# Performance work log

Hardware: AMD Instinct MI355X
Metric: run time of the kernel (lower is better)

The kernel has to match this reference:

```python
import jax, jax.numpy as jnp
import numpy as np

NEG = -9e15
SLOPE = 0.1  # LeakyReLU negative_slope in the torch module

B, N, NFEAT = 4, 2048, 256
NHID, NHEADS, NOUT = 64, 8, 128


def setup_inputs() -> dict:
    key = jax.random.key(0)
    ks = jax.random.split(key, 8)
    x = jax.random.normal(ks[0], (B, N, NFEAT), dtype=jnp.float32)
    adj = jax.random.randint(ks[1], (B, N, N), 0, 2, dtype=jnp.int32)
    s = 0.1
    Wh = jax.random.normal(ks[2], (NHEADS, NFEAT, NHID), dtype=jnp.float32) * s
    ah = jax.random.normal(ks[3], (NHEADS, 2 * NHID), dtype=jnp.float32) * s
    bh = jax.random.normal(ks[4], (NHEADS, NHID), dtype=jnp.float32) * s
    Wo = jax.random.normal(ks[5], (NHID * NHEADS, NOUT), dtype=jnp.float32) * s
    ao = jax.random.normal(ks[6], (2 * NOUT,), dtype=jnp.float32) * s
    bo = jax.random.normal(ks[7], (NOUT,), dtype=jnp.float32) * s
    return {"x": x, "adj": adj, "Wh": Wh, "ah": ah, "bh": bh,
            "Wo": Wo, "ao": ao, "bo": bo}


def _leaky(v):
    return jnp.where(v >= 0, v, SLOPE * v)


def _gat_layer(x, adj, W, a, b):
    # x: [B,N,Fin], W: [Fin,F], a: [2F], b: [F]
    h = jnp.einsum('bnf,fo->bno', x, W)          # [B,N,F]
    F = W.shape[1]
    a1, a2 = a[:F], a[F:]
    s1 = h @ a1                                   # [B,N] (query / row term)
    s2 = h @ a2                                   # [B,N] (key / col term)
    e = _leaky(s1[:, :, None] + s2[:, None, :])   # [B,N,N], avoids a_input blowup
    e = jnp.where(adj > 0, e, NEG)
    att = jax.nn.softmax(e, axis=2)               # [B,N,N]
    h_prime = jnp.einsum('bnm,bmf->bnf', att, h) + b
    return jax.nn.elu(h_prime)


def reference(x, adj, Wh, ah, bh, Wo, ao, bo):
    # per-head layers, vmapped over the head axis of the stacked params
    heads = jax.vmap(lambda W, a, b: _gat_layer(x, adj, W, a, b))(Wh, ah, bh)
    # [H,B,N,F] -> concat heads along feature dim: [B,N,H*F]
    hcat = jnp.transpose(heads, (1, 2, 0, 3)).reshape(x.shape[0], x.shape[1], -1)
    out = _gat_layer(hcat, adj, Wo, ao, bo)
    return jax.nn.relu(out)
```

## Files before the change

kernel.cpp:

```cpp
#include <hip/hip_runtime.h>

constexpr int B_ = 4;
constexpr int N_ = 2048;
constexpr int NFEAT_ = 256;
constexpr int NHEADS_ = 8;
constexpr float SLOPE_ = 0.1f;
constexpr float L2E = 1.4426950408889634f;

typedef __attribute__((ext_vector_type(8))) __fp16 f16x8;
typedef __attribute__((ext_vector_type(4))) __fp16 f16x4;
typedef __attribute__((ext_vector_type(2))) __fp16 f16x2;
typedef __attribute__((ext_vector_type(4))) float f32x4;
typedef __attribute__((ext_vector_type(2))) float f32x2;

__device__ __forceinline__ f16x8 pack8(const float* v) {
  union { f16x2 h2[4]; f16x8 h8; } u;
  u.h2[0] = __builtin_amdgcn_cvt_pkrtz(v[0], v[1]);
  u.h2[1] = __builtin_amdgcn_cvt_pkrtz(v[2], v[3]);
  u.h2[2] = __builtin_amdgcn_cvt_pkrtz(v[4], v[5]);
  u.h2[3] = __builtin_amdgcn_cvt_pkrtz(v[6], v[7]);
  return u.h8;
}
__device__ __forceinline__ f16x4 pack4(float a, float b, float c, float d) {
  union { f16x2 h2[2]; f16x4 h4; } u;
  u.h2[0] = __builtin_amdgcn_cvt_pkrtz(a, b);
  u.h2[1] = __builtin_amdgcn_cvt_pkrtz(c, d);
  return u.h4;
}

__device__ __forceinline__ unsigned int wpair(f32x2 p2, f32x2 s2p,
                                              f16x2 sl2, f16x2 cq2,
                                              unsigned int pm) {
  f32x2 z;
  asm("v_pk_add_f32 %0, %1, %2" : "=v"(z) : "v"(p2), "v"(s2p));
  f16x2 t0 = __builtin_amdgcn_cvt_pkrtz(z.x, z.y);
  f16x2 t1, tm;
  asm("v_pk_fma_f16 %0, %1, %2, %3" : "=v"(t1) : "v"(sl2), "v"(t0), "v"(cq2));
  asm("v_pk_max_f16 %0, %1, %2" : "=v"(tm) : "v"(t0), "v"(t1));
  unsigned int utm;
  __builtin_memcpy(&utm, &tm, 4);
  unsigned int hi, elo, ehi, pk;
  asm("v_lshrrev_b32 %0, 16, %1" : "=v"(hi) : "v"(utm));
  asm("v_exp_f16 %0, %1" : "=v"(elo) : "v"(utm));
  asm("v_exp_f16 %0, %1" : "=v"(ehi) : "v"(hi));
  asm("v_pack_b32_f16 %0, %1, %2" : "=v"(pk) : "v"(elo), "v"(ehi));
  return pk & pm;
}

__global__ __launch_bounds__(256) void k_prep(
    const int* __restrict__ adj, unsigned short* __restrict__ mask2,
    const float* __restrict__ Wh, __fp16* __restrict__ WhB,
    const float* __restrict__ Wo, __fp16* __restrict__ WoB)
{
  const int bid = blockIdx.x;
  const int l = threadIdx.x & 63;
  if (bid < 4096) {
    const size_t gw = ((size_t)bid * 256 + threadIdx.x) >> 6;
    const int jt = (int)(gw & 31);
    const int ig16 = (int)((gw >> 5) & 127);
    const int b = (int)(gw >> 12);
    const int q = l >> 4, c15 = l & 15;
    const int* base = adj + ((size_t)b * N_ + ig16 * 16) * N_ + jt * 64 + l;
    unsigned int msk = 0;
    #pragma unroll
    for (int r = 0; r < 16; ++r) {
      int a = base[(size_t)r * N_];
      unsigned long long bal = __ballot(a > 0);
      unsigned int v = (unsigned int)((bal >> (q * 8)) & 0xffull)
                     | ((unsigned int)((bal >> (q * 8 + 32)) & 0xffull) << 8);
      if (r == c15) msk = v;
    }
    mask2[gw * 64 + l] = (unsigned short)msk;
  } else if (bid < 4160) {
    int s = (int)(((bid - 4096) * 256 + threadIdx.x) >> 6);
    int h = s >> 5, ks = (s >> 2) & 7, ft = s & 3;
    const float* src = Wh + ((size_t)h * 256 + ks * 32 + (l >> 4) * 8) * 64 + ft * 16 + (l & 15);
    float v[8];
    #pragma unroll
    for (int j = 0; j < 8; ++j) v[j] = src[(size_t)j * 64];
    *(f16x8*)(WhB + (size_t)s * 512 + l * 8) = pack8(v);
  } else {
    int s = (int)(((bid - 4160) * 256 + threadIdx.x) >> 6);
    int ks = s >> 3, ft = s & 7;
    const float* src = Wo + ((size_t)ks * 32 + (l >> 4) * 8) * 128 + ft * 16 + (l & 15);
    float v[8];
    #pragma unroll
    for (int j = 0; j < 8; ++j) v[j] = src[(size_t)j * 128];
    *(f16x8*)(WoB + (size_t)s * 512 + l * 8) = pack8(v);
  }
}

__global__ __launch_bounds__(256, 4) void k_gemm1(
    const float* __restrict__ x, const __fp16* __restrict__ WhB,
    const float* __restrict__ ah,
    __fp16* __restrict__ hB1, float* __restrict__ s1h, float* __restrict__ s2h)
{
  constexpr int XP = 264;
  __shared__ __fp16 xs[16 * XP];
  __shared__ __fp16 hT[512 * 16];

  const int t = threadIdx.x;
  const int bid = blockIdx.x;
  const int b = bid >> 7;
  const int n0 = (bid & 127) * 16;

  {
    int r = t >> 4, k0 = (t & 15) * 16;
    const float* src = x + ((size_t)(b * N_) + n0 + r) * NFEAT_ + k0;
    float v0[8], v1[8];
    *(float4*)&v0[0] = *(const float4*)(src);
    *(float4*)&v0[4] = *(const float4*)(src + 4);
    *(float4*)&v1[0] = *(const float4*)(src + 8);
    *(float4*)&v1[4] = *(const float4*)(src + 12);
    *(f16x8*)&xs[r * XP + k0] = pack8(v0);
    *(f16x8*)&xs[r * XP + k0 + 8] = pack8(v1);
  }
  __syncthreads();

  const int w = t >> 6, l = t & 63;
  const int quad = l >> 4, c15 = l & 15;

  f32x4 acc[8];
  #pragma unroll
  for (int i = 0; i < 8; ++i) acc[i] = (f32x4){0.f, 0.f, 0.f, 0.f};

  for (int ks = 0; ks < 8; ++ks) {
    f16x8 af = *(const f16x8*)&xs[c15 * XP + ks * 32 + quad * 8];
    #pragma unroll
    for (int tt = 0; tt < 8; ++tt) {
      int hl = tt >> 2, ft = tt & 3;
      f16x8 bf = *(const f16x8*)(WhB +
          ((((size_t)(2 * w + hl) * 8 + ks) * 4 + ft) * 512) + l * 8);
      acc[tt] = __builtin_amdgcn_mfma_f32_16x16x32_f16(af, bf, acc[tt], 0, 0, 0);
    }
  }

  #pragma unroll
  for (int hl = 0; hl < 2; ++hl) {
    int head = 2 * w + hl;
    float a1v[4], a2v[4];
    #pragma unroll
    for (int ft = 0; ft < 4; ++ft) {
      a1v[ft] = ah[head * 128 + ft * 16 + c15] * L2E;
      a2v[ft] = ah[head * 128 + 64 + ft * 16 + c15] * L2E;
    }
    #pragma unroll
    for (int r = 0; r < 4; ++r) {
      float v1 = 0.f, v2 = 0.f;
      #pragma unroll
      for (int ft = 0; ft < 4; ++ft) {
        v1 = fmaf(acc[hl * 4 + ft][r], a1v[ft], v1);
        v2 = fmaf(acc[hl * 4 + ft][r], a2v[ft], v2);
      }
      #pragma unroll
      for (int off = 1; off < 16; off <<= 1) {
        v1 += __shfl_xor(v1, off, 64);
        v2 += __shfl_xor(v2, off, 64);
      }
      if (c15 == 0) {
        s1h[(size_t)(b * NHEADS_ + head) * N_ + n0 + quad * 4 + r] = v1;
        s2h[(size_t)(b * NHEADS_ + head) * N_ + n0 + quad * 4 + r] = v2;
      }
    }
  }

  #pragma unroll
  for (int tt = 0; tt < 8; ++tt) {
    int f = (2 * w + (tt >> 2)) * 64 + (tt & 3) * 16 + c15;
    *(f16x4*)&hT[f * 16 + quad * 4] =
        pack4(acc[tt][0], acc[tt][1], acc[tt][2], acc[tt][3]);
  }
  __syncthreads();

  const int base_oct = (n0 >> 3) & 3;
  #pragma unroll
  for (int q = 0; q < 4; ++q) {
    int s = t + q * 256;
    int c15v = s & 15, oct = (s >> 4) & 1, ft = (s >> 5) & 3, head = s >> 7;
    f16x8 v = *(const f16x8*)&hT[(head * 64 + ft * 16 + c15v) * 16 + oct * 8];
    int lane0 = (base_oct + oct) * 16 + c15v;
    *(f16x8*)(hB1 +
        ((((size_t)(b * NHEADS_ + head) * 64 + (n0 >> 5)) * 4 + ft) * 512) + lane0 * 8) = v;
  }
}

__global__ __launch_bounds__(256, 4) void k_gemm2(
    const __fp16* __restrict__ g1, const __fp16* __restrict__ WoB,
    const float* __restrict__ ao,
    __fp16* __restrict__ hB2, float* __restrict__ s1o, float* __restrict__ s2o)
{
  constexpr int GP = 520;
  __shared__ __fp16 gs[16 * GP];
  __shared__ __fp16 hT[128 * 16];
  __shared__ float sd1[4][16], sd2[4][16];

  const int t = threadIdx.x;
  const int bid = blockIdx.x;
  const int b = bid >> 7;
  const int n0 = (bid & 127) * 16;

  {
    int r = t >> 4, k0 = (t & 15) * 32;
    const __fp16* src = g1 + ((size_t)(b * N_) + n0 + r) * 512 + k0;
    #pragma unroll
    for (int i = 0; i < 4; ++i)
      *(f16x8*)&gs[r * GP + k0 + i * 8] = *(const f16x8*)(src + i * 8);
  }
  __syncthreads();

  const int w = t >> 6, l = t & 63;
  const int quad = l >> 4, c15 = l & 15;

  f32x4 acc[2];
  acc[0] = (f32x4){0.f, 0.f, 0.f, 0.f};
  acc[1] = (f32x4){0.f, 0.f, 0.f, 0.f};

  for (int ks = 0; ks < 16; ++ks) {
    f16x8 af = *(const f16x8*)&gs[c15 * GP + ks * 32 + quad * 8];
    #pragma unroll
    for (int tt = 0; tt < 2; ++tt) {
      int ft = 2 * w + tt;
      f16x8 bf = *(const f16x8*)(WoB + (((size_t)ks * 8 + ft) * 512) + l * 8);
      acc[tt] = __builtin_amdgcn_mfma_f32_16x16x32_f16(af, bf, acc[tt], 0, 0, 0);
    }
  }

  {
    float a1v[2], a2v[2];
    #pragma unroll
    for (int tt = 0; tt < 2; ++tt) {
      int f = (2 * w + tt) * 16 + c15;
      a1v[tt] = ao[f] * L2E;
      a2v[tt] = ao[128 + f] * L2E;
    }
    #pragma unroll
    for (int r = 0; r < 4; ++r) {
      float v1 = acc[0][r] * a1v[0] + acc[1][r] * a1v[1];
      float v2 = acc[0][r] * a2v[0] + acc[1][r] * a2v[1];
      #pragma unroll
      for (int off = 1; off < 16; off <<= 1) {
        v1 += __shfl_xor(v1, off, 64);
        v2 += __shfl_xor(v2, off, 64);
      }
      if (c15 == 0) { sd1[w][quad * 4 + r] = v1; sd2[w][quad * 4 + r] = v2; }
    }
  }

  #pragma unroll
  for (int tt = 0; tt < 2; ++tt) {
    int f = (2 * w + tt) * 16 + c15;
    *(f16x4*)&hT[f * 16 + quad * 4] =
        pack4(acc[tt][0], acc[tt][1], acc[tt][2], acc[tt][3]);
  }
  __syncthreads();

  if (t < 16)
    s1o[(size_t)b * N_ + n0 + t] = sd1[0][t] + sd1[1][t] + sd1[2][t] + sd1[3][t];
  else if (t < 32) {
    int rr = t - 16;
    s2o[(size_t)b * N_ + n0 + rr] = sd2[0][rr] + sd2[1][rr] + sd2[2][rr] + sd2[3][rr];
  }

  {
    int c15v = t & 15, oct = (t >> 4) & 1, ft = t >> 5;
    f16x8 v = *(const f16x8*)&hT[(ft * 16 + c15v) * 16 + oct * 8];
    int base_oct = (n0 >> 3) & 3;
    int lane0 = (base_oct + oct) * 16 + c15v;
    *(f16x8*)(hB2 +
        (((size_t)(b * 64 + (n0 >> 5)) * 8 + ft) * 512) + lane0 * 8) = v;
  }
}

__global__ __launch_bounds__(512, 4) void k_att1(
    const __fp16* __restrict__ hB, const float* __restrict__ s1,
    const float* __restrict__ s2, const unsigned short* __restrict__ mask2,
    const float* __restrict__ bias, __fp16* __restrict__ g1)
{
  constexpr int NRG = 4, NJQ = 2, JLEN = 1024, TJ = 32, NIT = JLEN / TJ;
  constexpr int TILE = TJ * 64;

  __shared__ __fp16 vbuf[NJQ][2][TILE];
  __shared__ float s2s[N_];
  __shared__ float red[8];
  __shared__ uint2 mlut[16];

  const int tid = threadIdx.x;
  const int w = tid >> 6, l = tid & 63;
  const int quad = l >> 4, c15 = l & 15;
  const int rowg = w % NRG, jq = w / NRG;
  const int tc = rowg * 64 + l;

  int idx = blockIdx.x;
  const int ig = idx & 31; idx >>= 5;
  const int head = idx & 7;
  const int b = idx >> 3;
  const int i0w = ig * 64 + rowg * 16;

  const float* s1p = s1 + (size_t)(b * 8 + head) * N_;
  const float* s2p = s2 + (size_t)(b * 8 + head) * N_;
  const char* hBp = (const char*)(hB + (size_t)(b * 8 + head) * (N_ / 32) * 2048);
  const unsigned short* mp = mask2 + ((size_t)(b * 128 + (i0w >> 4)) * 32) * 64 + l;

  const int jbase = jq * JLEN;

  if (tid < 16) {
    unsigned int v = tid;
    mlut[tid] = (uint2){ ((v & 1u) ? 0xffffu : 0u) | ((v & 2u) ? 0xffff0000u : 0u),
                         ((v & 4u) ? 0xffffu : 0u) | ((v & 8u) ? 0xffff0000u : 0u) };
  }

  float4 pf0 = *(const float4*)(hBp + (size_t)(jbase >> 5) * 4096 + tc * 16);
  unsigned short mk = mp[(size_t)(jbase >> 6) * 64];

  float4 sv = *(const float4*)(s2p + tid * 4);
  *(float4*)&s2s[tid * 4] = sv;
  float lm = fmaxf(fmaxf(sv.x, sv.y), fmaxf(sv.z, sv.w));
  #pragma unroll
  for (int off = 1; off < 64; off <<= 1) lm = fmaxf(lm, __shfl_xor(lm, off, 64));
  if (l == 0) red[w] = lm;
  const float s1v = s1p[i0w + c15];
  *(float4*)((char*)&vbuf[jq][0][0] + tc * 16) = pf0;
  __syncthreads();
  float s2m = red[0];
  #pragma unroll
  for (int q = 1; q < 8; ++q) s2m = fmaxf(s2m, red[q]);

  const float zm = s1v + s2m;
  const float m = fmaxf(zm, SLOPE_ * zm);
  const float p = s1v - m;
  const float cq = (SLOPE_ - 1.f) * m;
  const f16x2 cq2 = __builtin_amdgcn_cvt_pkrtz(cq, cq);
  const f16x2 sl2 = (f16x2){(__fp16)SLOPE_, (__fp16)SLOPE_};
  const f32x2 p2 = {p, p};

  f16x8 ones;
  #pragma unroll
  for (int i = 0; i < 8; ++i) ones[i] = (__fp16)1.0f;

  f32x4 acc[4], acc5;
  #pragma unroll
  for (int t = 0; t < 4; ++t) acc[t] = (f32x4){0.f, 0.f, 0.f, 0.f};
  acc5 = (f32x4){0.f, 0.f, 0.f, 0.f};

  for (int it = 0; it < NIT; ++it) {
    const int cur = it & 1;
    const int j0 = jbase + it * TJ;
    unsigned short nk = 0;
    float4 npf;
    if (it + 1 < NIT) {
      npf = *(const float4*)(hBp + (size_t)((j0 + TJ) >> 5) * 4096 + tc * 16);
      nk = mp[(size_t)((j0 + TJ) >> 6) * 64];
    }

    float4 sA = *(const float4*)&s2s[j0 + quad * 8];
    float4 sB = *(const float4*)&s2s[j0 + quad * 8 + 4];
    const unsigned int mbyte = ((unsigned int)mk >> (8 * ((j0 >> 5) & 1))) & 0xffu;
    const uint2 mA = mlut[mbyte & 15u];
    const uint2 mB = mlut[mbyte >> 4];
    union { unsigned int u[4]; f16x8 v8; } af;
    af.u[0] = wpair(p2, (f32x2){sA.x, sA.y}, sl2, cq2, mA.x);
    af.u[1] = wpair(p2, (f32x2){sA.z, sA.w}, sl2, cq2, mA.y);
    af.u[2] = wpair(p2, (f32x2){sB.x, sB.y}, sl2, cq2, mB.x);
    af.u[3] = wpair(p2, (f32x2){sB.z, sB.w}, sl2, cq2, mB.y);
    const f16x8 a = af.v8;
    acc5 = __builtin_amdgcn_mfma_f32_16x16x32_f16(a, ones, acc5, 0, 0, 0);
    const __fp16* vb = &vbuf[jq][cur][0];
    #pragma unroll
    for (int t = 0; t < 4; ++t) {
      f16x8 bf = *(const f16x8*)(vb + t * 512 + l * 8);
      acc[t] = __builtin_amdgcn_mfma_f32_16x16x32_f16(a, bf, acc[t], 0, 0, 0);
    }

    if (it + 1 < NIT) {
      *(float4*)((char*)&vbuf[jq][cur ^ 1][0] + tc * 16) = npf;
    }
    mk = nk;
    __syncthreads();
  }

  auto pacc = (float(*)[16][64])(&vbuf[0][0][0]);
  auto pls  = (float(*)[16])(&s2s[0]);
  if (jq == 1) {
    #pragma unroll
    for (int t = 0; t < 4; ++t)
      #pragma unroll
      for (int r = 0; r < 4; ++r)
        pacc[rowg][quad * 4 + r][t * 16 + c15] = acc[t][r];
    if (c15 == 0) {
      #pragma unroll
      for (int r = 0; r < 4; ++r) pls[rowg][quad * 4 + r] = acc5[r];
    }
  }
  __syncthreads();
  if (jq == 0) {
    float Lrow[4];
    #pragma unroll
    for (int r = 0; r < 4; ++r)
      Lrow[r] = acc5[r] + pls[rowg][quad * 4 + r];
    #pragma unroll
    for (int t = 0; t < 4; ++t)
      #pragma unroll
      for (int r = 0; r < 4; ++r)
        acc[t][r] += pacc[rowg][quad * 4 + r][t * 16 + c15];
    float lr[4];
    #pragma unroll
    for (int r = 0; r < 4; ++r) lr[r] = 1.f / Lrow[r];
    #pragma unroll
    for (int t = 0; t < 4; ++t) {
      const float bv = bias[head * 64 + t * 16 + c15];
      #pragma unroll
      for (int r = 0; r < 4; ++r) {
        const int i = i0w + quad * 4 + r;
        float v = acc[t][r] * lr[r] + bv;
        v = (v > 0.f) ? v : expm1f(v);
        g1[(size_t)(b * N_ + i) * 512 + head * 64 + t * 16 + c15] = (__fp16)v;
      }
    }
  }
}

__global__ __launch_bounds__(512, 4) void k_att2(
    const __fp16* __restrict__ hB, const float* __restrict__ s1,
    const float* __restrict__ s2, const unsigned short* __restrict__ mask2,
    const float* __restrict__ bias, float* __restrict__ out)
{
  constexpr int NRG = 2, NJQ = 4, JLEN = 512, TJ = 32, NIT = JLEN / TJ;
  constexpr int TILE = TJ * 64;

  __shared__ __fp16 vbuf[NJQ][2][TILE];
  __shared__ float s2s[N_];
  __shared__ float red[8];
  __shared__ uint2 mlut[16];

  const int tid = threadIdx.x;
  const int w = tid >> 6, l = tid & 63;
  const int quad = l >> 4, c15 = l & 15;
  const int rowg = w % NRG, jq = w / NRG;
  const int tc = rowg * 64 + l;

  int idx = blockIdx.x;
  const int ig = idx & 63; idx >>= 6;
  const int fs = idx & 1;
  const int b = idx >> 1;
  const int i0w = ig * 32 + rowg * 16;

  const float* s1p = s1 + (size_t)b * N_;
  const float* s2p = s2 + (size_t)b * N_;
  const char* hBp = (const char*)(hB + (size_t)b * 64 * 4096 + fs * 2048);
  const unsigned short* mp = mask2 + ((size_t)(b * 128 + (i0w >> 4)) * 32) * 64 + l;

  const int jbase = jq * JLEN;

  if (tid < 16) {
    unsigned int v = tid;
    mlut[tid] = (uint2){ ((v & 1u) ? 0xffffu : 0u) | ((v & 2u) ? 0xffff0000u : 0u),
                         ((v & 4u) ? 0xffffu : 0u) | ((v & 8u) ? 0xffff0000u : 0u) };
  }

  float4 pf0, pf1;
  {
    const char* srcb = hBp + (size_t)(jbase >> 5) * 8192;
    pf0 = *(const float4*)(srcb + tc * 16);
    pf1 = *(const float4*)(srcb + (tc + 128) * 16);
  }
  unsigned short mk = mp[(size_t)(jbase >> 6) * 64];

  float4 sv = *(const float4*)(s2p + tid * 4);
  *(float4*)&s2s[tid * 4] = sv;
  float lm = fmaxf(fmaxf(sv.x, sv.y), fmaxf(sv.z, sv.w));
  #pragma unroll
  for (int off = 1; off < 64; off <<= 1) lm = fmaxf(lm, __shfl_xor(lm, off, 64));
  if (l == 0) red[w] = lm;
  const float s1v = s1p[i0w + c15];
  *(float4*)((char*)&vbuf[jq][0][0] + tc * 16) = pf0;
  *(float4*)((char*)&vbuf[jq][0][0] + (tc + 128) * 16) = pf1;
  __syncthreads();
  float s2m = red[0];
  #pragma unroll
  for (int q = 1; q < 8; ++q) s2m = fmaxf(s2m, red[q]);

  const float zm = s1v + s2m;
  const float m = fmaxf(zm, SLOPE_ * zm);
  const float p = s1v - m;
  const float cq = (SLOPE_ - 1.f) * m;
  const f16x2 cq2 = __builtin_amdgcn_cvt_pkrtz(cq, cq);
  const f16x2 sl2 = (f16x2){(__fp16)SLOPE_, (__fp16)SLOPE_};
  const f32x2 p2 = {p, p};

  f16x8 ones;
  #pragma unroll
  for (int i = 0; i < 8; ++i) ones[i] = (__fp16)1.0f;

  f32x4 acc[4], acc5;
  #pragma unroll
  for (int t = 0; t < 4; ++t) acc[t] = (f32x4){0.f, 0.f, 0.f, 0.f};
  acc5 = (f32x4){0.f, 0.f, 0.f, 0.f};

  for (int it = 0; it < NIT; ++it) {
    const int cur = it & 1;
    const int j0 = jbase + it * TJ;
    unsigned short nk = 0;
    float4 npf0, npf1;
    if (it + 1 < NIT) {
      const char* srcb = hBp + (size_t)((j0 + TJ) >> 5) * 8192;
      npf0 = *(const float4*)(srcb + tc * 16);
      npf1 = *(const float4*)(srcb + (tc + 128) * 16);
      nk = mp[(size_t)((j0 + TJ) >> 6) * 64];
    }

    float4 sA = *(const float4*)&s2s[j0 + quad * 8];
    float4 sB = *(const float4*)&s2s[j0 + quad * 8 + 4];
    const unsigned int mbyte = ((unsigned int)mk >> (8 * ((j0 >> 5) & 1))) & 0xffu;
    const uint2 mA = mlut[mbyte & 15u];
    const uint2 mB = mlut[mbyte >> 4];
    union { unsigned int u[4]; f16x8 v8; } af;
    af.u[0] = wpair(p2, (f32x2){sA.x, sA.y}, sl2, cq2, mA.x);
    af.u[1] = wpair(p2, (f32x2){sA.z, sA.w}, sl2, cq2, mA.y);
    af.u[2] = wpair(p2, (f32x2){sB.x, sB.y}, sl2, cq2, mB.x);
    af.u[3] = wpair(p2, (f32x2){sB.z, sB.w}, sl2, cq2, mB.y);
    const f16x8 a = af.v8;
    acc5 = __builtin_amdgcn_mfma_f32_16x16x32_f16(a, ones, acc5, 0, 0, 0);
    const __fp16* vb = &vbuf[jq][cur][0];
    #pragma unroll
    for (int t = 0; t < 4; ++t) {
      f16x8 bf = *(const f16x8*)(vb + t * 512 + l * 8);
      acc[t] = __builtin_amdgcn_mfma_f32_16x16x32_f16(a, bf, acc[t], 0, 0, 0);
    }

    if (it + 1 < NIT) {
      char* dst = (char*)&vbuf[jq][cur ^ 1][0];
      *(float4*)(dst + tc * 16) = npf0;
      *(float4*)(dst + (tc + 128) * 16) = npf1;
    }
    mk = nk;
    __syncthreads();
  }

  auto pacc = (float(*)[NRG][16][64])(&vbuf[0][0][0]);
  auto pls  = (float(*)[NRG][16])(&s2s[0]);
  if (jq > 0) {
    #pragma unroll
    for (int t = 0; t < 4; ++t)
      #pragma unroll
      for (int r = 0; r < 4; ++r)
        pacc[jq - 1][rowg][quad * 4 + r][t * 16 + c15] = acc[t][r];
    if (c15 == 0) {
      #pragma unroll
      for (int r = 0; r < 4; ++r) pls[jq - 1][rowg][quad * 4 + r] = acc5[r];
    }
  }
  __syncthreads();
  if (jq == 0) {
    float Lrow[4];
    #pragma unroll
    for (int r = 0; r < 4; ++r) Lrow[r] = acc5[r];
    #pragma unroll
    for (int q = 0; q < NJQ - 1; ++q) {
      #pragma unroll
      for (int t = 0; t < 4; ++t)
        #pragma unroll
        for (int r = 0; r < 4; ++r)
          acc[t][r] += pacc[q][rowg][quad * 4 + r][t * 16 + c15];
      #pragma unroll
      for (int r = 0; r < 4; ++r) Lrow[r] += pls[q][rowg][quad * 4 + r];
    }
    float lr[4];
    #pragma unroll
    for (int r = 0; r < 4; ++r) lr[r] = 1.f / Lrow[r];
    #pragma unroll
    for (int t = 0; t < 4; ++t) {
      const float bv = bias[fs * 64 + t * 16 + c15];
      #pragma unroll
      for (int r = 0; r < 4; ++r) {
        const int i = i0w + quad * 4 + r;
        float v = acc[t][r] * lr[r] + bv;
        out[(size_t)(b * N_ + i) * 128 + fs * 64 + t * 16 + c15] = fmaxf(v, 0.f);
      }
    }
  }
}

extern "C" void kernel_launch(void* const* d_in, const int* in_sizes, int n_in,
                              void* d_out, int out_size, void* d_ws, size_t ws_size,
                              hipStream_t stream) {
  const float* x   = (const float*)d_in[0];
  const int*   adj = (const int*)d_in[1];
  const float* Wh  = (const float*)d_in[2];
  const float* ah  = (const float*)d_in[3];
  const float* bh  = (const float*)d_in[4];
  const float* Wo  = (const float*)d_in[5];
  const float* ao  = (const float*)d_in[6];
  const float* bo  = (const float*)d_in[7];
  float* out = (float*)d_out;

  float* ws   = (float*)d_ws;
  float* s1h  = ws;
  float* s2h  = s1h  + (size_t)B_ * NHEADS_ * N_;
  float* s1o  = s2h  + (size_t)B_ * NHEADS_ * N_;
  float* s2o  = s1o  + (size_t)B_ * N_;
  __fp16* g1  = (__fp16*)(s2o + (size_t)B_ * N_);
  __fp16* hB1 = g1  + (size_t)B_ * N_ * 512;
  __fp16* hB2 = hB1 + (size_t)B_ * NHEADS_ * N_ * 64;
  __fp16* WhB = hB2 + (size_t)B_ * N_ * 128;
  __fp16* WoB = WhB + (size_t)8 * 256 * 64;
  unsigned short* mask2 = (unsigned short*)(WoB + (size_t)512 * 128);

  k_prep<<<4192, 256, 0, stream>>>(adj, mask2, Wh, WhB, Wo, WoB);
  k_gemm1<<<B_ * (N_ / 16), 256, 0, stream>>>(x, WhB, ah, hB1, s1h, s2h);
  k_att1<<<B_ * NHEADS_ * (N_ / 64), 512, 0, stream>>>(
      hB1, s1h, s2h, mask2, bh, g1);
  k_gemm2<<<B_ * (N_ / 16), 256, 0, stream>>>(g1, WoB, ao, hB2, s1o, s2o);
  k_att2<<<B_ * 2 * (N_ / 32), 512, 0, stream>>>(
      hB2, s1o, s2o, mask2, bo, out);
}
```

Baseline: 194.0 us.

## Factor leaky-softmax exponent into per-row and per-column exp products

The attention kernels no longer evaluate exp(leaky(s1+s2)-m) per element. They precompute exp(s2) and exp(slope*s2) per column in fp16 inside the GEMM kernels, and per-row factors exp(s1-m) and exp(slope*s1-m). The inner loop then forms each weight as the max of two packed fp16 products, using monotonicity of exp. The global column max now comes from atomicMax on order-preserving encoded floats, which removes the in-block reduction. k_att1 doubles its j-tile and both attention kernels prefetch the value tile two iterations ahead. This trades per-element exp work for fp16 products whose factors may underflow or overflow, and adds a dependency on atomics that are zeroed in k_prep.

```diff
diff --git a/kernel.cpp b/kernel.cpp
--- a/kernel.cpp
+++ b/kernel.cpp
@@ -11,7 +11,6 @@
 typedef __attribute__((ext_vector_type(4))) __fp16 f16x4;
 typedef __attribute__((ext_vector_type(2))) __fp16 f16x2;
 typedef __attribute__((ext_vector_type(4))) float f32x4;
-typedef __attribute__((ext_vector_type(2))) float f32x2;
 
 __device__ __forceinline__ f16x8 pack8(const float* v) {
   union { f16x2 h2[4]; f16x8 h8; } u;
@@ -28,29 +27,34 @@
   return u.h4;
 }
 
-__device__ __forceinline__ unsigned int wpair(f32x2 p2, f32x2 s2p,
-                                              f16x2 sl2, f16x2 cq2,
-                                              unsigned int pm) {
-  f32x2 z;
-  asm("v_pk_add_f32 %0, %1, %2" : "=v"(z) : "v"(p2), "v"(s2p));
-  f16x2 t0 = __builtin_amdgcn_cvt_pkrtz(z.x, z.y);
-  f16x2 t1, tm;
-  asm("v_pk_fma_f16 %0, %1, %2, %3" : "=v"(t1) : "v"(sl2), "v"(t0), "v"(cq2));
-  asm("v_pk_max_f16 %0, %1, %2" : "=v"(tm) : "v"(t0), "v"(t1));
-  unsigned int utm;
-  __builtin_memcpy(&utm, &tm, 4);
-  unsigned int hi, elo, ehi, pk;
-  asm("v_lshrrev_b32 %0, 16, %1" : "=v"(hi) : "v"(utm));
-  asm("v_exp_f16 %0, %1" : "=v"(elo) : "v"(utm));
-  asm("v_exp_f16 %0, %1" : "=v"(ehi) : "v"(hi));
-  asm("v_pack_b32_f16 %0, %1, %2" : "=v"(pk) : "v"(elo), "v"(ehi));
-  return pk & pm;
+__device__ __forceinline__ unsigned int fenc(float x) {
+  int i = __float_as_int(x);
+  return (i >= 0) ? ((unsigned int)i | 0x80000000u) : (unsigned int)(~i);
+}
+__device__ __forceinline__ float fdec(unsigned int k) {
+  int i = (k & 0x80000000u) ? (int)(k & 0x7fffffffu) : ~(int)k;
+  return __int_as_float(i);
+}
+
+__device__ __forceinline__ unsigned int wmax(f16x2 Ep2, f16x2 Eq2,
+                                             unsigned int e1p, unsigned int e2p) {
+  f16x2 ea, eb;
+  __builtin_memcpy(&ea, &e1p, 4);
+  __builtin_memcpy(&eb, &e2p, 4);
+  f16x2 a, b, c;
+  asm("v_pk_mul_f16 %0, %1, %2" : "=v"(a) : "v"(Ep2), "v"(ea));
+  asm("v_pk_mul_f16 %0, %1, %2" : "=v"(b) : "v"(Eq2), "v"(eb));
+  asm("v_pk_max_f16 %0, %1, %2" : "=v"(c) : "v"(a), "v"(b));
+  unsigned int r;
+  __builtin_memcpy(&r, &c, 4);
+  return r;
 }
 
 __global__ __launch_bounds__(256) void k_prep(
     const int* __restrict__ adj, unsigned short* __restrict__ mask2,
     const float* __restrict__ Wh, __fp16* __restrict__ WhB,
-    const float* __restrict__ Wo, __fp16* __restrict__ WoB)
+    const float* __restrict__ Wo, __fp16* __restrict__ WoB,
+    unsigned int* __restrict__ mxb)
 {
   const int bid = blockIdx.x;
   const int l = threadIdx.x & 63;
@@ -80,6 +84,7 @@
     for (int j = 0; j < 8; ++j) v[j] = src[(size_t)j * 64];
     *(f16x8*)(WhB + (size_t)s * 512 + l * 8) = pack8(v);
   } else {
+    if (bid == 4191 && threadIdx.x < 36) mxb[threadIdx.x] = 0u;
     int s = (int)(((bid - 4160) * 256 + threadIdx.x) >> 6);
     int ks = s >> 3, ft = s & 7;
     const float* src = Wo + ((size_t)ks * 32 + (l >> 4) * 8) * 128 + ft * 16 + (l & 15);
@@ -93,7 +98,9 @@
 __global__ __launch_bounds__(256, 4) void k_gemm1(
     const float* __restrict__ x, const __fp16* __restrict__ WhB,
     const float* __restrict__ ah,
-    __fp16* __restrict__ hB1, float* __restrict__ s1h, float* __restrict__ s2h)
+    __fp16* __restrict__ hB1, float* __restrict__ s1h,
+    __fp16* __restrict__ e1h, __fp16* __restrict__ e2h,
+    unsigned int* __restrict__ mxb)
 {
   constexpr int XP = 264;
   __shared__ __fp16 xs[16 * XP];
@@ -144,6 +151,7 @@
       a1v[ft] = ah[head * 128 + ft * 16 + c15] * L2E;
       a2v[ft] = ah[head * 128 + 64 + ft * 16 + c15] * L2E;
     }
+    float hmax = -1e30f;
     #pragma unroll
     for (int r = 0; r < 4; ++r) {
       float v1 = 0.f, v2 = 0.f;
@@ -158,10 +166,16 @@
         v2 += __shfl_xor(v2, off, 64);
       }
       if (c15 == 0) {
-        s1h[(size_t)(b * NHEADS_ + head) * N_ + n0 + quad * 4 + r] = v1;
-        s2h[(size_t)(b * NHEADS_ + head) * N_ + n0 + quad * 4 + r] = v2;
+        const size_t nn = (size_t)(b * NHEADS_ + head) * N_ + n0 + quad * 4 + r;
+        s1h[nn] = v1;
+        e1h[nn] = (__fp16)__builtin_amdgcn_exp2f(v2);
+        e2h[nn] = (__fp16)__builtin_amdgcn_exp2f(SLOPE_ * v2);
       }
-    }
+      hmax = fmaxf(hmax, v2);
+    }
+    hmax = fmaxf(hmax, __shfl_xor(hmax, 16, 64));
+    hmax = fmaxf(hmax, __shfl_xor(hmax, 32, 64));
+    if (l == 0) atomicMax(&mxb[b * NHEADS_ + head], fenc(hmax));
   }
 
   #pragma unroll
@@ -187,7 +201,9 @@
 __global__ __launch_bounds__(256, 4) void k_gemm2(
     const __fp16* __restrict__ g1, const __fp16* __restrict__ WoB,
     const float* __restrict__ ao,
-    __fp16* __restrict__ hB2, float* __restrict__ s1o, float* __restrict__ s2o)
+    __fp16* __restrict__ hB2, float* __restrict__ s1o,
+    __fp16* __restrict__ e1o, __fp16* __restrict__ e2o,
+    unsigned int* __restrict__ mxb)
 {
   constexpr int GP = 520;
   __shared__ __fp16 gs[16 * GP];
@@ -258,7 +274,15 @@
     s1o[(size_t)b * N_ + n0 + t] = sd1[0][t] + sd1[1][t] + sd1[2][t] + sd1[3][t];
   else if (t < 32) {
     int rr = t - 16;
-    s2o[(size_t)b * N_ + n0 + rr] = sd2[0][rr] + sd2[1][rr] + sd2[2][rr] + sd2[3][rr];
+    float v = sd2[0][rr] + sd2[1][rr] + sd2[2][rr] + sd2[3][rr];
+    e1o[(size_t)b * N_ + n0 + rr] = (__fp16)__builtin_amdgcn_exp2f(v);
+    e2o[(size_t)b * N_ + n0 + rr] = (__fp16)__builtin_amdgcn_exp2f(SLOPE_ * v);
+    float hm = v;
+    hm = fmaxf(hm, __shfl_xor(hm, 1, 64));
+    hm = fmaxf(hm, __shfl_xor(hm, 2, 64));
+    hm = fmaxf(hm, __shfl_xor(hm, 4, 64));
+    hm = fmaxf(hm, __shfl_xor(hm, 8, 64));
+    if (rr == 0) atomicMax(&mxb[32 + b], fenc(hm));
   }
 
   {
@@ -273,15 +297,16 @@
 
 __global__ __launch_bounds__(512, 4) void k_att1(
     const __fp16* __restrict__ hB, const float* __restrict__ s1,
-    const float* __restrict__ s2, const unsigned short* __restrict__ mask2,
+    const __fp16* __restrict__ e1, const __fp16* __restrict__ e2,
+    const unsigned int* __restrict__ mxb,
+    const unsigned short* __restrict__ mask2,
     const float* __restrict__ bias, __fp16* __restrict__ g1)
 {
-  constexpr int NRG = 4, NJQ = 2, JLEN = 1024, TJ = 32, NIT = JLEN / TJ;
+  constexpr int NRG = 4, NJQ = 2, JLEN = 1024, TJ = 64, NIT = JLEN / TJ;
   constexpr int TILE = TJ * 64;
 
   __shared__ __fp16 vbuf[NJQ][2][TILE];
-  __shared__ float s2s[N_];
-  __shared__ float red[8];
+  __shared__ __fp16 ets[2][N_];
   __shared__ uint2 mlut[16];
 
   const int tid = threadIdx.x;
@@ -295,10 +320,10 @@
   const int head = idx & 7;
   const int b = idx >> 3;
   const int i0w = ig * 64 + rowg * 16;
-
-  const float* s1p = s1 + (size_t)(b * 8 + head) * N_;
-  const float* s2p = s2 + (size_t)(b * 8 + head) * N_;
-  const char* hBp = (const char*)(hB + (size_t)(b * 8 + head) * (N_ / 32) * 2048);
+  const int bh = b * NHEADS_ + head;
+
+  const float* s1p = s1 + (size_t)bh * N_;
+  const char* hBp = (const char*)(hB + (size_t)bh * (N_ / 32) * 2048);
   const unsigned short* mp = mask2 + ((size_t)(b * 128 + (i0w >> 4)) * 32) * 64 + l;
 
   const int jbase = jq * JLEN;
@@ -309,29 +334,30 @@
                          ((v & 4u) ? 0xffffu : 0u) | ((v & 8u) ? 0xffff0000u : 0u) };
   }
 
-  float4 pf0 = *(const float4*)(hBp + (size_t)(jbase >> 5) * 4096 + tc * 16);
+  float4 pA0 = *(const float4*)(hBp + (size_t)(jbase >> 5) * 4096 + tc * 16);
+  float4 pA1 = *(const float4*)(hBp + (size_t)(jbase >> 5) * 4096 + (tc + 256) * 16);
+  float4 pB0 = *(const float4*)(hBp + (size_t)((jbase + TJ) >> 5) * 4096 + tc * 16);
+  float4 pB1 = *(const float4*)(hBp + (size_t)((jbase + TJ) >> 5) * 4096 + (tc + 256) * 16);
   unsigned short mk = mp[(size_t)(jbase >> 6) * 64];
 
-  float4 sv = *(const float4*)(s2p + tid * 4);
-  *(float4*)&s2s[tid * 4] = sv;
-  float lm = fmaxf(fmaxf(sv.x, sv.y), fmaxf(sv.z, sv.w));
-  #pragma unroll
-  for (int off = 1; off < 64; off <<= 1) lm = fmaxf(lm, __shfl_xor(lm, off, 64));
-  if (l == 0) red[w] = lm;
+  {
+    const int half = tid >> 8, off = (tid & 255) * 8;
+    const __fp16* src = (half ? e2 : e1) + (size_t)bh * N_ + off;
+    *(f16x8*)&ets[half][off] = *(const f16x8*)src;
+  }
+
   const float s1v = s1p[i0w + c15];
-  *(float4*)((char*)&vbuf[jq][0][0] + tc * 16) = pf0;
-  __syncthreads();
-  float s2m = red[0];
-  #pragma unroll
-  for (int q = 1; q < 8; ++q) s2m = fmaxf(s2m, red[q]);
+  const float s2m = fdec(mxb[bh]);
+  *(float4*)((char*)&vbuf[jq][0][0] + tc * 16) = pA0;
+  *(float4*)((char*)&vbuf[jq][0][0] + (tc + 256) * 16) = pA1;
+  __syncthreads();
 
   const float zm = s1v + s2m;
   const float m = fmaxf(zm, SLOPE_ * zm);
-  const float p = s1v - m;
-  const float cq = (SLOPE_ - 1.f) * m;
-  const f16x2 cq2 = __builtin_amdgcn_cvt_pkrtz(cq, cq);
-  const f16x2 sl2 = (f16x2){(__fp16)SLOPE_, (__fp16)SLOPE_};
-  const f32x2 p2 = {p, p};
+  const float Ep = __builtin_amdgcn_exp2f(s1v - m);
+  const float Eq = __builtin_amdgcn_exp2f(SLOPE_ * s1v - m);
+  const f16x2 Ep2 = __builtin_amdgcn_cvt_pkrtz(Ep, Ep);
+  const f16x2 Eq2 = __builtin_amdgcn_cvt_pkrtz(Eq, Eq);
 
   f16x8 ones;
   #pragma unroll
@@ -345,41 +371,45 @@
   for (int it = 0; it < NIT; ++it) {
     const int cur = it & 1;
     const int j0 = jbase + it * TJ;
+    if (it + 1 < NIT) {
+      *(float4*)((char*)&vbuf[jq][cur ^ 1][0] + tc * 16) = pB0;
+      *(float4*)((char*)&vbuf[jq][cur ^ 1][0] + (tc + 256) * 16) = pB1;
+    }
+    if (it + 2 < NIT) {
+      pB0 = *(const float4*)(hBp + (size_t)((j0 + 2 * TJ) >> 5) * 4096 + tc * 16);
+      pB1 = *(const float4*)(hBp + (size_t)((j0 + 2 * TJ) >> 5) * 4096 + (tc + 256) * 16);
+    }
     unsigned short nk = 0;
-    float4 npf;
-    if (it + 1 < NIT) {
-      npf = *(const float4*)(hBp + (size_t)((j0 + TJ) >> 5) * 4096 + tc * 16);
-      nk = mp[(size_t)((j0 + TJ) >> 6) * 64];
-    }
-
-    float4 sA = *(const float4*)&s2s[j0 + quad * 8];
-    float4 sB = *(const float4*)&s2s[j0 + quad * 8 + 4];
-    const unsigned int mbyte = ((unsigned int)mk >> (8 * ((j0 >> 5) & 1))) & 0xffu;
-    const uint2 mA = mlut[mbyte & 15u];
-    const uint2 mB = mlut[mbyte >> 4];
-    union { unsigned int u[4]; f16x8 v8; } af;
-    af.u[0] = wpair(p2, (f32x2){sA.x, sA.y}, sl2, cq2, mA.x);
-    af.u[1] = wpair(p2, (f32x2){sA.z, sA.w}, sl2, cq2, mA.y);
-    af.u[2] = wpair(p2, (f32x2){sB.x, sB.y}, sl2, cq2, mB.x);
-    af.u[3] = wpair(p2, (f32x2){sB.z, sB.w}, sl2, cq2, mB.y);
-    const f16x8 a = af.v8;
-    acc5 = __builtin_amdgcn_mfma_f32_16x16x32_f16(a, ones, acc5, 0, 0, 0);
-    const __fp16* vb = &vbuf[jq][cur][0];
-    #pragma unroll
-    for (int t = 0; t < 4; ++t) {
-      f16x8 bf = *(const f16x8*)(vb + t * 512 + l * 8);
-      acc[t] = __builtin_amdgcn_mfma_f32_16x16x32_f16(a, bf, acc[t], 0, 0, 0);
-    }
-
-    if (it + 1 < NIT) {
-      *(float4*)((char*)&vbuf[jq][cur ^ 1][0] + tc * 16) = npf;
+    if (it + 1 < NIT) nk = mp[(size_t)((j0 + TJ) >> 6) * 64];
+
+    #pragma unroll
+    for (int h = 0; h < 2; ++h) {
+      const int jk = j0 + h * 32;
+      uint4 e1u = *(const uint4*)((const char*)&ets[0][jk] + quad * 16);
+      uint4 e2u = *(const uint4*)((const char*)&ets[1][jk] + quad * 16);
+      const unsigned int mbyte = ((unsigned int)mk >> (8 * h)) & 0xffu;
+      const uint2 mA = mlut[mbyte & 15u];
+      const uint2 mB = mlut[mbyte >> 4];
+      union { unsigned int u[4]; f16x8 v8; } af;
+      af.u[0] = wmax(Ep2, Eq2, e1u.x, e2u.x) & mA.x;
+      af.u[1] = wmax(Ep2, Eq2, e1u.y, e2u.y) & mA.y;
+      af.u[2] = wmax(Ep2, Eq2, e1u.z, e2u.z) & mB.x;
+      af.u[3] = wmax(Ep2, Eq2, e1u.w, e2u.w) & mB.y;
+      const f16x8 a = af.v8;
+      acc5 = __builtin_amdgcn_mfma_f32_16x16x32_f16(a, ones, acc5, 0, 0, 0);
+      const __fp16* vb = &vbuf[jq][cur][h * 2048];
+      #pragma unroll
+      for (int t = 0; t < 4; ++t) {
+        f16x8 bf = *(const f16x8*)(vb + t * 512 + l * 8);
+        acc[t] = __builtin_amdgcn_mfma_f32_16x16x32_f16(a, bf, acc[t], 0, 0, 0);
+      }
     }
     mk = nk;
     __syncthreads();
   }
 
   auto pacc = (float(*)[16][64])(&vbuf[0][0][0]);
-  auto pls  = (float(*)[16])(&s2s[0]);
+  auto pls  = (float(*)[16])((char*)&vbuf[0][0][0] + 16384);
   if (jq == 1) {
     #pragma unroll
     for (int t = 0; t < 4; ++t)
@@ -421,15 +451,16 @@
 
 __global__ __launch_bounds__(512, 4) void k_att2(
     const __fp16* __restrict__ hB, const float* __restrict__ s1,
-    const float* __restrict__ s2, const unsigned short* __restrict__ mask2,
+    const __fp16* __restrict__ e1, const __fp16* __restrict__ e2,
+    const unsigned int* __restrict__ mxb,
+    const unsigned short* __restrict__ mask2,
     const float* __restrict__ bias, float* __restrict__ out)
 {
   constexpr int NRG = 2, NJQ = 4, JLEN = 512, TJ = 32, NIT = JLEN / TJ;
   constexpr int TILE = TJ * 64;
 
   __shared__ __fp16 vbuf[NJQ][2][TILE];
-  __shared__ float s2s[N_];
-  __shared__ float red[8];
+  __shared__ __fp16 ets[2][N_];
   __shared__ uint2 mlut[16];
 
   const int tid = threadIdx.x;
@@ -445,7 +476,6 @@
   const int i0w = ig * 32 + rowg * 16;
 
   const float* s1p = s1 + (size_t)b * N_;
-  const float* s2p = s2 + (size_t)b * N_;
   const char* hBp = (const char*)(hB + (size_t)b * 64 * 4096 + fs * 2048);
   const unsigned short* mp = mask2 + ((size_t)(b * 128 + (i0w >> 4)) * 32) * 64 + l;
 
@@ -457,35 +487,30 @@
                          ((v & 4u) ? 0xffffu : 0u) | ((v & 8u) ? 0xffff0000u : 0u) };
   }
 
-  float4 pf0, pf1;
+  float4 pA0 = *(const float4*)(hBp + (size_t)(jbase >> 5) * 8192 + tc * 16);
+  float4 pA1 = *(const float4*)(hBp + (size_t)(jbase >> 5) * 8192 + (tc + 128) * 16);
+  float4 pB0 = *(const float4*)(hBp + (size_t)((jbase + TJ) >> 5) * 8192 + tc * 16);
+  float4 pB1 = *(const float4*)(hBp + (size_t)((jbase + TJ) >> 5) * 8192 + (tc + 128) * 16);
+  unsigned short mk = mp[(size_t)(jbase >> 6) * 64];
+
   {
-    const char* srcb = hBp + (size_t)(jbase >> 5) * 8192;
-    pf0 = *(const float4*)(srcb + tc * 16);
-    pf1 = *(const float4*)(srcb + (tc + 128) * 16);
-  }
-  unsigned short mk = mp[(size_t)(jbase >> 6) * 64];
-
-  float4 sv = *(const float4*)(s2p + tid * 4);
-  *(float4*)&s2s[tid * 4] = sv;
-  float lm = fmaxf(fmaxf(sv.x, sv.y), fmaxf(sv.z, sv.w));
-  #pragma unroll
-  for (int off = 1; off < 64; off <<= 1) lm = fmaxf(lm, __shfl_xor(lm, off, 64));
-  if (l == 0) red[w] = lm;
+    const int half = tid >> 8, off = (tid & 255) * 8;
+    const __fp16* src = (half ? e2 : e1) + (size_t)b * N_ + off;
+    *(f16x8*)&ets[half][off] = *(const f16x8*)src;
+  }
+
   const float s1v = s1p[i0w + c15];
-  *(float4*)((char*)&vbuf[jq][0][0] + tc * 16) = pf0;
-  *(float4*)((char*)&vbuf[jq][0][0] + (tc + 128) * 16) = pf1;
-  __syncthreads();
-  float s2m = red[0];
-  #pragma unroll
-  for (int q = 1; q < 8; ++q) s2m = fmaxf(s2m, red[q]);
+  const float s2m = fdec(mxb[32 + b]);
+  *(float4*)((char*)&vbuf[jq][0][0] + tc * 16) = pA0;
+  *(float4*)((char*)&vbuf[jq][0][0] + (tc + 128) * 16) = pA1;
+  __syncthreads();
 
   const float zm = s1v + s2m;
   const float m = fmaxf(zm, SLOPE_ * zm);
-  const float p = s1v - m;
-  const float cq = (SLOPE_ - 1.f) * m;
-  const f16x2 cq2 = __builtin_amdgcn_cvt_pkrtz(cq, cq);
-  const f16x2 sl2 = (f16x2){(__fp16)SLOPE_, (__fp16)SLOPE_};
-  const f32x2 p2 = {p, p};
+  const float Ep = __builtin_amdgcn_exp2f(s1v - m);
+  const float Eq = __builtin_amdgcn_exp2f(SLOPE_ * s1v - m);
+  const f16x2 Ep2 = __builtin_amdgcn_cvt_pkrtz(Ep, Ep);
+  const f16x2 Eq2 = __builtin_amdgcn_cvt_pkrtz(Eq, Eq);
 
   f16x8 ones;
   #pragma unroll
@@ -499,25 +524,27 @@
   for (int it = 0; it < NIT; ++it) {
     const int cur = it & 1;
     const int j0 = jbase + it * TJ;
+    if (it + 1 < NIT) {
+      *(float4*)((char*)&vbuf[jq][cur ^ 1][0] + tc * 16) = pB0;
+      *(float4*)((char*)&vbuf[jq][cur ^ 1][0] + (tc + 128) * 16) = pB1;
+    }
+    if (it + 2 < NIT) {
+      pB0 = *(const float4*)(hBp + (size_t)((j0 + 2 * TJ) >> 5) * 8192 + tc * 16);
+      pB1 = *(const float4*)(hBp + (size_t)((j0 + 2 * TJ) >> 5) * 8192 + (tc + 128) * 16);
+    }
     unsigned short nk = 0;
-    float4 npf0, npf1;
-    if (it + 1 < NIT) {
-      const char* srcb = hBp + (size_t)((j0 + TJ) >> 5) * 8192;
-      npf0 = *(const float4*)(srcb + tc * 16);
-      npf1 = *(const float4*)(srcb + (tc + 128) * 16);
-      nk = mp[(size_t)((j0 + TJ) >> 6) * 64];
-    }
-
-    float4 sA = *(const float4*)&s2s[j0 + quad * 8];
-    float4 sB = *(const float4*)&s2s[j0 + quad * 8 + 4];
+    if (it + 1 < NIT) nk = mp[(size_t)((j0 + TJ) >> 6) * 64];
+
+    uint4 e1u = *(const uint4*)((const char*)&ets[0][j0] + quad * 16);
+    uint4 e2u = *(const uint4*)((const char*)&ets[1][j0] + quad * 16);
     const unsigned int mbyte = ((unsigned int)mk >> (8 * ((j0 >> 5) & 1))) & 0xffu;
     const uint2 mA = mlut[mbyte & 15u];
     const uint2 mB = mlut[mbyte >> 4];
     union { unsigned int u[4]; f16x8 v8; } af;
-    af.u[0] = wpair(p2, (f32x2){sA.x, sA.y}, sl2, cq2, mA.x);
-    af.u[1] = wpair(p2, (f32x2){sA.z, sA.w}, sl2, cq2, mA.y);
-    af.u[2] = wpair(p2, (f32x2){sB.x, sB.y}, sl2, cq2, mB.x);
-    af.u[3] = wpair(p2, (f32x2){sB.z, sB.w}, sl2, cq2, mB.y);
+    af.u[0] = wmax(Ep2, Eq2, e1u.x, e2u.x) & mA.x;
+    af.u[1] = wmax(Ep2, Eq2, e1u.y, e2u.y) & mA.y;
+    af.u[2] = wmax(Ep2, Eq2, e1u.z, e2u.z) & mB.x;
+    af.u[3] = wmax(Ep2, Eq2, e1u.w, e2u.w) & mB.y;
     const f16x8 a = af.v8;
     acc5 = __builtin_amdgcn_mfma_f32_16x16x32_f16(a, ones, acc5, 0, 0, 0);
     const __fp16* vb = &vbuf[jq][cur][0];
@@ -526,18 +553,12 @@
       f16x8 bf = *(const f16x8*)(vb + t * 512 + l * 8);
       acc[t] = __builtin_amdgcn_mfma_f32_16x16x32_f16(a, bf, acc[t], 0, 0, 0);
     }
-
-    if (it + 1 < NIT) {
-      char* dst = (char*)&vbuf[jq][cur ^ 1][0];
-      *(float4*)(dst + tc * 16) = npf0;
-      *(float4*)(dst + (tc + 128) * 16) = npf1;
-    }
     mk = nk;
     __syncthreads();
   }
 
   auto pacc = (float(*)[NRG][16][64])(&vbuf[0][0][0]);
-  auto pls  = (float(*)[NRG][16])(&s2s[0]);
+  auto pls  = (float(*)[NRG][16])((char*)&vbuf[0][0][0] + 24576);
   if (jq > 0) {
     #pragma unroll
     for (int t = 0; t < 4; ++t)
@@ -604,12 +625,17 @@
   __fp16* WhB = hB2 + (size_t)B_ * N_ * 128;
   __fp16* WoB = WhB + (size_t)8 * 256 * 64;
   unsigned short* mask2 = (unsigned short*)(WoB + (size_t)512 * 128);
-
-  k_prep<<<4192, 256, 0, stream>>>(adj, mask2, Wh, WhB, Wo, WoB);
-  k_gemm1<<<B_ * (N_ / 16), 256, 0, stream>>>(x, WhB, ah, hB1, s1h, s2h);
+  __fp16* e1h = (__fp16*)(mask2 + (size_t)B_ * 128 * 32 * 64);
+  __fp16* e2h = e1h + (size_t)B_ * NHEADS_ * N_;
+  __fp16* e1o = e2h + (size_t)B_ * NHEADS_ * N_;
+  __fp16* e2o = e1o + (size_t)B_ * N_;
+  unsigned int* mxb = (unsigned int*)(e2o + (size_t)B_ * N_);
+
+  k_prep<<<4192, 256, 0, stream>>>(adj, mask2, Wh, WhB, Wo, WoB, mxb);
+  k_gemm1<<<B_ * (N_ / 16), 256, 0, stream>>>(x, WhB, ah, hB1, s1h, e1h, e2h, mxb);
   k_att1<<<B_ * NHEADS_ * (N_ / 64), 512, 0, stream>>>(
-      hB1, s1h, s2h, mask2, bh, g1);
-  k_gemm2<<<B_ * (N_ / 16), 256, 0, stream>>>(g1, WoB, ao, hB2, s1o, s2o);
+      hB1, s1h, e1h, e2h, mxb, mask2, bh, g1);
+  k_gemm2<<<B_ * (N_ / 16), 256, 0, stream>>>(g1, WoB, ao, hB2, s1o, e1o, e2o, mxb);
   k_att2<<<B_ * 2 * (N_ / 32), 512, 0, stream>>>(
-      hB2, s1o, s2o, mask2, bo, out);
-}
+      hB2, s1o, e1o, e2o, mxb, mask2, bo, out);
+}
```

Result: slower. 217.0 us (+11.9%).
